# Kernel optimization log

Hardware: AMD Instinct MI355X
Metric: run time of the kernel (lower is better)

The kernel has to match this reference:

```python
import jax, jax.numpy as jnp
import numpy as np
from jax import lax

KX = jnp.array([[-1., 0., 1.], [-2., 0., 2.], [-1., 0., 1.]], dtype=jnp.float32)
KY = jnp.array([[1., 2., 1.], [0., 0., 0.], [-1., -2., -1.]], dtype=jnp.float32)


def _dwconv3(x, k):
    # x: [B,C,H,W]; k: [3,3]; depthwise 3x3 cross-correlation, padding=1 (matches torch F.conv2d)
    C = x.shape[1]
    kern = jnp.broadcast_to(k.astype(x.dtype)[None, None], (C, 1, 3, 3))
    return lax.conv_general_dilated(
        x, kern, window_strides=(1, 1), padding='SAME',
        dimension_numbers=('NCHW', 'OIHW', 'NCHW'), feature_group_count=C)


def _sobel(x):
    # |sobel_x| + |sobel_y|, shape [B,C,H,W] (the original adds a size-1 K dim, squeezed/kept trivially)
    return jnp.abs(_dwconv3(x, KX)) + jnp.abs(_dwconv3(x, KY))


def setup_inputs() -> dict:
    key = jax.random.key(0)
    ks = jax.random.split(key, 4)
    shape = (16, 1, 768, 768)
    return {
        'image_vis': jax.random.uniform(ks[0], shape, dtype=jnp.float32),
        'image_ir': jax.random.uniform(ks[1], shape, dtype=jnp.float32),
        'image_X': jax.random.uniform(ks[2], shape, dtype=jnp.float32),
        'image_Y': jax.random.uniform(ks[3], shape, dtype=jnp.float32),
    }


def reference(image_vis, image_ir, image_X, image_Y):
    # loss_in = mean(sobel(Y)^2) / mean(sobel(X)^2)
    x_size = jnp.mean(jnp.square(_sobel(image_X)))
    y_size = jnp.mean(jnp.square(_sobel(image_Y)))
    loss_in = y_size / x_size

    y_grad = _sobel(image_vis)
    ir_grad = _sobel(image_ir)          # broadcast replaces .expand
    gen_grad = _sobel(image_X)
    joint = jnp.maximum(y_grad, ir_grad)
    loss_grad = jnp.mean(jnp.abs(gen_grad - joint))  # F.l1_loss
    return (loss_in, loss_grad)
```

## Files before the change

### kernel.cpp

```cpp
#include <hip/hip_runtime.h>
#include <math.h>

#define IMG_H 768
#define IMG_W 768
#define BATCH 16
#define TH 4
#define TPB 256
#define NSTRIPS (IMG_H / TH)
#define NBLOCKS (NSTRIPS * BATCH)
#define NPIX ((size_t)BATCH * IMG_H * IMG_W)

typedef const __attribute__((address_space(1))) float* gp1_t;
typedef __attribute__((address_space(3))) float* lp3_t;

__global__ __launch_bounds__(TPB) void sobel_loss_main(
    const float* __restrict__ vis, const float* __restrict__ ir,
    const float* __restrict__ X, const float* __restrict__ Y,
    float* __restrict__ part)
{
    __shared__ __align__(16) float lds[4][TH + 2][IMG_W];
    __shared__ float red[3][4];

    const int tid  = threadIdx.x;
    const int lane = tid & 63;
    const int wv   = tid >> 6;
    const int y0   = blockIdx.x * TH;
    const size_t base = (size_t)blockIdx.y * (IMG_H * IMG_W);
    const int bid = blockIdx.y * NSTRIPS + blockIdx.x;

    const float* img[4] = { vis + base, ir + base, X + base, Y + base };

    {
        const float* ip = img[wv];
        #pragma unroll
        for (int i = 0; i < 3 * (TH + 2); ++i) {
            const int row = i / 3, seg = i % 3;
            int gr = y0 - 1 + row;
            int rc = gr < 0 ? 0 : (gr > IMG_H - 1 ? IMG_H - 1 : gr);
            const float* src = ip + (size_t)rc * IMG_W + seg * 256 + lane * 4;
            __builtin_amdgcn_global_load_lds((gp1_t)src, (lp3_t)&lds[wv][row][seg * 256], 16, 0, 0);
        }
    }
    __syncthreads();

    if (y0 == 0) {
        for (int i = tid; i < IMG_W; i += TPB) {
            lds[0][0][i] = 0.f; lds[1][0][i] = 0.f; lds[2][0][i] = 0.f; lds[3][0][i] = 0.f;
        }
        __syncthreads();
    } else if (y0 + TH == IMG_H) {
        for (int i = tid; i < IMG_W; i += TPB) {
            lds[0][TH + 1][i] = 0.f; lds[1][TH + 1][i] = 0.f; lds[2][TH + 1][i] = 0.f; lds[3][TH + 1][i] = 0.f;
        }
        __syncthreads();
    }

    const int r0 = wv, r1 = wv + 1, r2 = wv + 2;
    const int xb = lane * 12;

    float jnt[12];
    float sX2 = 0.f, sY2 = 0.f, sL1 = 0.f;

    #pragma unroll
    for (int im = 0; im < 4; ++im) {
        float4 t0 = *(const float4*)&lds[im][r0][xb];
        float4 t1 = *(const float4*)&lds[im][r0][xb + 4];
        float4 t2 = *(const float4*)&lds[im][r0][xb + 8];
        float4 m0 = *(const float4*)&lds[im][r1][xb];
        float4 m1 = *(const float4*)&lds[im][r1][xb + 4];
        float4 m2 = *(const float4*)&lds[im][r1][xb + 8];
        float4 b0 = *(const float4*)&lds[im][r2][xb];
        float4 b1 = *(const float4*)&lds[im][r2][xb + 4];
        float4 b2 = *(const float4*)&lds[im][r2][xb + 8];

        float T[14], M[14], B[14];
        T[1] = t0.x; T[2] = t0.y; T[3] = t0.z; T[4] = t0.w;
        T[5] = t1.x; T[6] = t1.y; T[7] = t1.z; T[8] = t1.w;
        T[9] = t2.x; T[10] = t2.y; T[11] = t2.z; T[12] = t2.w;
        M[1] = m0.x; M[2] = m0.y; M[3] = m0.z; M[4] = m0.w;
        M[5] = m1.x; M[6] = m1.y; M[7] = m1.z; M[8] = m1.w;
        M[9] = m2.x; M[10] = m2.y; M[11] = m2.z; M[12] = m2.w;
        B[1] = b0.x; B[2] = b0.y; B[3] = b0.z; B[4] = b0.w;
        B[5] = b1.x; B[6] = b1.y; B[7] = b1.z; B[8] = b1.w;
        B[9] = b2.x; B[10] = b2.y; B[11] = b2.z; B[12] = b2.w;

        float tl = __shfl_up(t2.w, 1),  tr = __shfl_down(t0.x, 1);
        float ml = __shfl_up(m2.w, 1),  mr = __shfl_down(m0.x, 1);
        float bl = __shfl_up(b2.w, 1),  br = __shfl_down(b0.x, 1);
        T[0] = (lane == 0) ? 0.f : tl;  T[13] = (lane == 63) ? 0.f : tr;
        M[0] = (lane == 0) ? 0.f : ml;  M[13] = (lane == 63) ? 0.f : mr;
        B[0] = (lane == 0) ? 0.f : bl;  B[13] = (lane == 63) ? 0.f : br;

        float s[14], d[14];
        #pragma unroll
        for (int j = 0; j < 14; ++j) { s[j] = T[j] + B[j]; d[j] = T[j] - B[j]; }

        float g[12];
        #pragma unroll
        for (int j = 0; j < 12; ++j) {
            float gx = (s[j + 2] - s[j]) + 2.f * (M[j + 2] - M[j]);
            float gy = d[j] + 2.f * d[j + 1] + d[j + 2];
            g[j] = fabsf(gx) + fabsf(gy);
        }

        if (im == 0) {
            #pragma unroll
            for (int j = 0; j < 12; ++j) jnt[j] = g[j];
        } else if (im == 1) {
            #pragma unroll
            for (int j = 0; j < 12; ++j) jnt[j] = fmaxf(jnt[j], g[j]);
        } else if (im == 2) {
            #pragma unroll
            for (int j = 0; j < 12; ++j) {
                sX2 += g[j] * g[j];
                sL1 += fabsf(g[j] - jnt[j]);
            }
        } else {
            #pragma unroll
            for (int j = 0; j < 12; ++j) sY2 += g[j] * g[j];
        }
    }

    #pragma unroll
    for (int off = 32; off > 0; off >>= 1) {
        sX2 += __shfl_down(sX2, off);
        sY2 += __shfl_down(sY2, off);
        sL1 += __shfl_down(sL1, off);
    }
    if (lane == 0) { red[0][wv] = sX2; red[1][wv] = sY2; red[2][wv] = sL1; }
    __syncthreads();
    if (tid == 0) {
        part[0 * NBLOCKS + bid] = red[0][0] + red[0][1] + red[0][2] + red[0][3];
        part[1 * NBLOCKS + bid] = red[1][0] + red[1][1] + red[1][2] + red[1][3];
        part[2 * NBLOCKS + bid] = red[2][0] + red[2][1] + red[2][2] + red[2][3];
    }
}

__global__ __launch_bounds__(1024) void reduce_finalize(
    const float* __restrict__ part, float* __restrict__ out)
{
    __shared__ float red[3][16];
    const int tid = threadIdx.x;

    float a = 0.f, b = 0.f, c = 0.f;
    for (int i = tid; i < NBLOCKS; i += 1024) {
        a += part[0 * NBLOCKS + i];
        b += part[1 * NBLOCKS + i];
        c += part[2 * NBLOCKS + i];
    }
    #pragma unroll
    for (int off = 32; off > 0; off >>= 1) {
        a += __shfl_down(a, off);
        b += __shfl_down(b, off);
        c += __shfl_down(c, off);
    }
    const int wave = tid >> 6;
    const int lane = tid & 63;
    if (lane == 0) { red[0][wave] = a; red[1][wave] = b; red[2][wave] = c; }
    __syncthreads();
    if (tid == 0) {
        float sa = 0.f, sb = 0.f, sc = 0.f;
        #pragma unroll
        for (int w = 0; w < 16; ++w) { sa += red[0][w]; sb += red[1][w]; sc += red[2][w]; }
        out[0] = sb / sa;
        out[1] = sc * (1.f / (float)NPIX);
    }
}

extern "C" void kernel_launch(void* const* d_in, const int* in_sizes, int n_in,
                              void* d_out, int out_size, void* d_ws, size_t ws_size,
                              hipStream_t stream) {
    const float* vis = (const float*)d_in[0];
    const float* ir  = (const float*)d_in[1];
    const float* X   = (const float*)d_in[2];
    const float* Y   = (const float*)d_in[3];
    float* out = (float*)d_out;
    float* part = (float*)d_ws;

    dim3 grid(NSTRIPS, BATCH);
    sobel_loss_main<<<grid, TPB, 0, stream>>>(vis, ir, X, Y, part);
    reduce_finalize<<<1, 1024, 0, stream>>>(part, out);
}
```

Baseline: 41.48 us.

## Persistent blocks with double-buffered LDS staging and fused last-block reduction

Replaces the one-strip-per-block grid with 256 persistent blocks that each process 12 strips. Staging uses two LDS buffers, so global-to-LDS loads for the next strip overlap computation on the current one, coordinated with manual vmcnt waits and barriers. The separate finalize kernel is replaced by an atomic counter, and the last finishing block performs the final reduction. This adds a memset launch and doubles LDS per block (about 147KB), which limits occupancy to one block per CU, and the inline waitcnt values have to be exactly right for correctness.

```diff
diff --git a/kernel.cpp b/kernel.cpp
--- a/kernel.cpp
+++ b/kernel.cpp
@@ -6,72 +6,48 @@
 #define BATCH 16
 #define TH 4
 #define TPB 256
-#define NSTRIPS (IMG_H / TH)
-#define NBLOCKS (NSTRIPS * BATCH)
+#define NBLK 256
+#define SPB 12
 #define NPIX ((size_t)BATCH * IMG_H * IMG_W)
 
 typedef const __attribute__((address_space(1))) float* gp1_t;
 typedef __attribute__((address_space(3))) float* lp3_t;
 
-__global__ __launch_bounds__(TPB) void sobel_loss_main(
-    const float* __restrict__ vis, const float* __restrict__ ir,
-    const float* __restrict__ X, const float* __restrict__ Y,
-    float* __restrict__ part)
-{
-    __shared__ __align__(16) float lds[4][TH + 2][IMG_W];
-    __shared__ float red[3][4];
-
-    const int tid  = threadIdx.x;
-    const int lane = tid & 63;
-    const int wv   = tid >> 6;
-    const int y0   = blockIdx.x * TH;
-    const size_t base = (size_t)blockIdx.y * (IMG_H * IMG_W);
-    const int bid = blockIdx.y * NSTRIPS + blockIdx.x;
-
-    const float* img[4] = { vis + base, ir + base, X + base, Y + base };
-
-    {
-        const float* ip = img[wv];
-        #pragma unroll
-        for (int i = 0; i < 3 * (TH + 2); ++i) {
-            const int row = i / 3, seg = i % 3;
-            int gr = y0 - 1 + row;
-            int rc = gr < 0 ? 0 : (gr > IMG_H - 1 ? IMG_H - 1 : gr);
-            const float* src = ip + (size_t)rc * IMG_W + seg * 256 + lane * 4;
-            __builtin_amdgcn_global_load_lds((gp1_t)src, (lp3_t)&lds[wv][row][seg * 256], 16, 0, 0);
-        }
-    }
-    __syncthreads();
-
-    if (y0 == 0) {
-        for (int i = tid; i < IMG_W; i += TPB) {
-            lds[0][0][i] = 0.f; lds[1][0][i] = 0.f; lds[2][0][i] = 0.f; lds[3][0][i] = 0.f;
-        }
-        __syncthreads();
-    } else if (y0 + TH == IMG_H) {
-        for (int i = tid; i < IMG_W; i += TPB) {
-            lds[0][TH + 1][i] = 0.f; lds[1][TH + 1][i] = 0.f; lds[2][TH + 1][i] = 0.f; lds[3][TH + 1][i] = 0.f;
-        }
-        __syncthreads();
-    }
-
+#define SBAR()   __builtin_amdgcn_s_barrier()
+#define SCHEDB() __builtin_amdgcn_sched_barrier(0)
+#define WAIT_VM18() asm volatile("s_waitcnt vmcnt(18)" ::: "memory")
+#define WAIT_VM0()  asm volatile("s_waitcnt vmcnt(0)"  ::: "memory")
+#define WAIT_LGKM0() asm volatile("s_waitcnt lgkmcnt(0)" ::: "memory")
+
+__device__ __forceinline__ void stage_img(const float* __restrict__ ip,
+                                          float (*buf)[IMG_W], int y0, int lane) {
+    #pragma unroll
+    for (int i = 0; i < 18; ++i) {
+        const int row = i / 3, seg = i % 3;
+        int gr = y0 - 1 + row;
+        int rc = gr < 0 ? 0 : (gr > IMG_H - 1 ? IMG_H - 1 : gr);
+        const float* src = ip + (size_t)rc * IMG_W + seg * 256 + lane * 4;
+        __builtin_amdgcn_global_load_lds((gp1_t)src, (lp3_t)&buf[row][seg * 256], 16, 0, 0);
+    }
+}
+
+__device__ __forceinline__ void compute_strip(const float (*buf)[TH + 2][IMG_W],
+                                              int wv, int lane,
+                                              float& sX2, float& sY2, float& sL1) {
     const int r0 = wv, r1 = wv + 1, r2 = wv + 2;
     const int xb = lane * 12;
-
     float jnt[12];
-    float sX2 = 0.f, sY2 = 0.f, sL1 = 0.f;
-
     #pragma unroll
     for (int im = 0; im < 4; ++im) {
-        float4 t0 = *(const float4*)&lds[im][r0][xb];
-        float4 t1 = *(const float4*)&lds[im][r0][xb + 4];
-        float4 t2 = *(const float4*)&lds[im][r0][xb + 8];
-        float4 m0 = *(const float4*)&lds[im][r1][xb];
-        float4 m1 = *(const float4*)&lds[im][r1][xb + 4];
-        float4 m2 = *(const float4*)&lds[im][r1][xb + 8];
-        float4 b0 = *(const float4*)&lds[im][r2][xb];
-        float4 b1 = *(const float4*)&lds[im][r2][xb + 4];
-        float4 b2 = *(const float4*)&lds[im][r2][xb + 8];
+        float4 t0 = *(const float4*)&buf[im][r0][xb];
+        float4 t1 = *(const float4*)&buf[im][r0][xb + 4];
+        float4 t2 = *(const float4*)&buf[im][r0][xb + 8];
+        float4 m0 = *(const float4*)&buf[im][r1][xb];
+        float4 m1 = *(const float4*)&buf[im][r1][xb + 4];
+        float4 m2 = *(const float4*)&buf[im][r1][xb + 8];
+        float4 b0 = *(const float4*)&buf[im][r2][xb];
+        float4 b1 = *(const float4*)&buf[im][r2][xb + 4];
+        float4 b2 = *(const float4*)&buf[im][r2][xb + 8];
 
         float T[14], M[14], B[14];
         T[1] = t0.x; T[2] = t0.y; T[3] = t0.z; T[4] = t0.w;
@@ -102,7 +78,6 @@
             float gy = d[j] + 2.f * d[j + 1] + d[j + 2];
             g[j] = fabsf(gx) + fabsf(gy);
         }
-
         if (im == 0) {
             #pragma unroll
             for (int j = 0; j < 12; ++j) jnt[j] = g[j];
@@ -111,14 +86,67 @@
             for (int j = 0; j < 12; ++j) jnt[j] = fmaxf(jnt[j], g[j]);
         } else if (im == 2) {
             #pragma unroll
-            for (int j = 0; j < 12; ++j) {
-                sX2 += g[j] * g[j];
-                sL1 += fabsf(g[j] - jnt[j]);
-            }
+            for (int j = 0; j < 12; ++j) { sX2 += g[j] * g[j]; sL1 += fabsf(g[j] - jnt[j]); }
         } else {
             #pragma unroll
             for (int j = 0; j < 12; ++j) sY2 += g[j] * g[j];
         }
+    }
+}
+
+__global__ __launch_bounds__(TPB) void sobel_loss_fused(
+    const float* __restrict__ vis, const float* __restrict__ ir,
+    const float* __restrict__ X, const float* __restrict__ Y,
+    float* __restrict__ part, unsigned* __restrict__ counter,
+    float* __restrict__ out)
+{
+    __shared__ __align__(16) float bufA[4][TH + 2][IMG_W];
+    __shared__ __align__(16) float bufB[4][TH + 2][IMG_W];
+    __shared__ float red[3][4];
+    __shared__ int lastLds;
+
+    const int tid  = threadIdx.x;
+    const int lane = tid & 63;
+    const int wv   = tid >> 6;
+    const int b    = blockIdx.x;
+    const int ib   = b >> 4;
+    const int ys0  = (b & 15) * SPB;
+    const size_t base = (size_t)ib * (IMG_H * IMG_W);
+    const float* img0[4] = { vis + base, ir + base, X + base, Y + base };
+    const float* ip = img0[wv];
+
+    float sX2 = 0.f, sY2 = 0.f, sL1 = 0.f;
+
+    stage_img(ip, bufA[wv], ys0 * TH, lane);
+
+    #pragma unroll 1
+    for (int t = 0; t < SPB / 2; ++t) {
+        const int y0A = (ys0 + 2 * t) * TH;
+        const int y0B = y0A + TH;
+
+        stage_img(ip, bufB[wv], y0B, lane);
+        WAIT_VM18();
+        SBAR(); SCHEDB();
+        if (y0A == 0) {
+            for (int i = tid; i < 4 * IMG_W; i += TPB) bufA[i / IMG_W][0][i % IMG_W] = 0.f;
+            WAIT_LGKM0(); SBAR();
+        }
+        compute_strip((const float (*)[TH + 2][IMG_W])bufA, wv, lane, sX2, sY2, sL1);
+        SCHEDB(); SBAR();
+
+        if (t < SPB / 2 - 1) {
+            stage_img(ip, bufA[wv], y0B + TH, lane);
+            WAIT_VM18();
+        } else {
+            WAIT_VM0();
+        }
+        SBAR(); SCHEDB();
+        if (y0B + TH == IMG_H) {
+            for (int i = tid; i < 4 * IMG_W; i += TPB) bufB[i / IMG_W][TH + 1][i % IMG_W] = 0.f;
+            WAIT_LGKM0(); SBAR();
+        }
+        compute_strip((const float (*)[TH + 2][IMG_W])bufB, wv, lane, sX2, sY2, sL1);
+        SCHEDB(); SBAR();
     }
 
     #pragma unroll
@@ -130,40 +158,35 @@
     if (lane == 0) { red[0][wv] = sX2; red[1][wv] = sY2; red[2][wv] = sL1; }
     __syncthreads();
     if (tid == 0) {
-        part[0 * NBLOCKS + bid] = red[0][0] + red[0][1] + red[0][2] + red[0][3];
-        part[1 * NBLOCKS + bid] = red[1][0] + red[1][1] + red[1][2] + red[1][3];
-        part[2 * NBLOCKS + bid] = red[2][0] + red[2][1] + red[2][2] + red[2][3];
-    }
-}
-
-__global__ __launch_bounds__(1024) void reduce_finalize(
-    const float* __restrict__ part, float* __restrict__ out)
-{
-    __shared__ float red[3][16];
-    const int tid = threadIdx.x;
-
-    float a = 0.f, b = 0.f, c = 0.f;
-    for (int i = tid; i < NBLOCKS; i += 1024) {
-        a += part[0 * NBLOCKS + i];
-        b += part[1 * NBLOCKS + i];
-        c += part[2 * NBLOCKS + i];
-    }
-    #pragma unroll
-    for (int off = 32; off > 0; off >>= 1) {
-        a += __shfl_down(a, off);
-        b += __shfl_down(b, off);
-        c += __shfl_down(c, off);
-    }
-    const int wave = tid >> 6;
-    const int lane = tid & 63;
-    if (lane == 0) { red[0][wave] = a; red[1][wave] = b; red[2][wave] = c; }
+        part[0 * NBLK + b] = red[0][0] + red[0][1] + red[0][2] + red[0][3];
+        part[1 * NBLK + b] = red[1][0] + red[1][1] + red[1][2] + red[1][3];
+        part[2 * NBLK + b] = red[2][0] + red[2][1] + red[2][2] + red[2][3];
+        __threadfence();
+        unsigned tk = atomicAdd(counter, 1u);
+        lastLds = (tk == NBLK - 1);
+    }
     __syncthreads();
-    if (tid == 0) {
-        float sa = 0.f, sb = 0.f, sc = 0.f;
+
+    if (lastLds) {
+        __threadfence();
+        float a = part[0 * NBLK + tid];
+        float c2 = part[1 * NBLK + tid];
+        float c3 = part[2 * NBLK + tid];
         #pragma unroll
-        for (int w = 0; w < 16; ++w) { sa += red[0][w]; sb += red[1][w]; sc += red[2][w]; }
-        out[0] = sb / sa;
-        out[1] = sc * (1.f / (float)NPIX);
+        for (int off = 32; off > 0; off >>= 1) {
+            a  += __shfl_down(a,  off);
+            c2 += __shfl_down(c2, off);
+            c3 += __shfl_down(c3, off);
+        }
+        if (lane == 0) { red[0][wv] = a; red[1][wv] = c2; red[2][wv] = c3; }
+        __syncthreads();
+        if (tid == 0) {
+            float sa = red[0][0] + red[0][1] + red[0][2] + red[0][3];
+            float sb = red[1][0] + red[1][1] + red[1][2] + red[1][3];
+            float sc = red[2][0] + red[2][1] + red[2][2] + red[2][3];
+            out[0] = sb / sa;
+            out[1] = sc * (1.f / (float)NPIX);
+        }
     }
 }
 
@@ -175,9 +198,10 @@
     const float* X   = (const float*)d_in[2];
     const float* Y   = (const float*)d_in[3];
     float* out = (float*)d_out;
-    float* part = (float*)d_ws;
-
-    dim3 grid(NSTRIPS, BATCH);
-    sobel_loss_main<<<grid, TPB, 0, stream>>>(vis, ir, X, Y, part);
-    reduce_finalize<<<1, 1024, 0, stream>>>(part, out);
-}
+
+    unsigned* counter = (unsigned*)d_ws;
+    float* part = (float*)((char*)d_ws + 256);
+
+    hipMemsetAsync(counter, 0, sizeof(unsigned), stream);
+    sobel_loss_fused<<<NBLK, TPB, 0, stream>>>(vis, ir, X, Y, part, counter, out);
+}
```

Measured after the change: 47.12 us. 13.6% more time.

## Fuse final reduction into main kernel via atomic counter and double strip height

Applied to the files above, without the earlier changes.

The separate finalize kernel is folded into the main kernel: each block writes its partial sums, bumps a global atomic counter, and the last block to finish reduces all partials and writes the outputs. Strip height goes from 4 to 8 rows with 512 threads per block, so the halo overhead per block is smaller and there are half as many blocks and partials. A memset of the counter is added before the launch. The larger LDS footprint (about 120 KB per block) may lower occupancy.

```diff
diff --git a/kernel.cpp b/kernel.cpp
--- a/kernel.cpp
+++ b/kernel.cpp
@@ -4,8 +4,8 @@
 #define IMG_H 768
 #define IMG_W 768
 #define BATCH 16
-#define TH 4
-#define TPB 256
+#define TH 8
+#define TPB 512
 #define NSTRIPS (IMG_H / TH)
 #define NBLOCKS (NSTRIPS * BATCH)
 #define NPIX ((size_t)BATCH * IMG_H * IMG_W)
@@ -13,13 +13,15 @@
 typedef const __attribute__((address_space(1))) float* gp1_t;
 typedef __attribute__((address_space(3))) float* lp3_t;
 
-__global__ __launch_bounds__(TPB) void sobel_loss_main(
+__global__ __launch_bounds__(TPB) void sobel_loss_fused(
     const float* __restrict__ vis, const float* __restrict__ ir,
     const float* __restrict__ X, const float* __restrict__ Y,
-    float* __restrict__ part)
+    float* __restrict__ part, unsigned* __restrict__ counter,
+    float* __restrict__ out)
 {
-    __shared__ __align__(16) float lds[4][TH + 2][IMG_W];
-    __shared__ float red[3][4];
+    __shared__ __align__(16) float buf[4][TH + 2][IMG_W];
+    __shared__ float red[3][8];
+    __shared__ int lastLds;
 
     const int tid  = threadIdx.x;
     const int lane = tid & 63;
@@ -28,30 +30,32 @@
     const size_t base = (size_t)blockIdx.y * (IMG_H * IMG_W);
     const int bid = blockIdx.y * NSTRIPS + blockIdx.x;
 
-    const float* img[4] = { vis + base, ir + base, X + base, Y + base };
-
     {
-        const float* ip = img[wv];
+        const int im = wv >> 1;
+        const float* ip = (im == 0) ? vis : (im == 1) ? ir : (im == 2) ? X : Y;
+        ip += base;
+        const int half = wv & 1;
         #pragma unroll
-        for (int i = 0; i < 3 * (TH + 2); ++i) {
-            const int row = i / 3, seg = i % 3;
+        for (int i = 0; i < 15; ++i) {
+            const int idx = half * 15 + i;
+            const int row = idx / 3, seg = idx % 3;
             int gr = y0 - 1 + row;
             int rc = gr < 0 ? 0 : (gr > IMG_H - 1 ? IMG_H - 1 : gr);
             const float* src = ip + (size_t)rc * IMG_W + seg * 256 + lane * 4;
-            __builtin_amdgcn_global_load_lds((gp1_t)src, (lp3_t)&lds[wv][row][seg * 256], 16, 0, 0);
+            __builtin_amdgcn_global_load_lds((gp1_t)src, (lp3_t)&buf[im][row][seg * 256], 16, 0, 0);
         }
     }
     __syncthreads();
 
-    if (y0 == 0) {
-        for (int i = tid; i < IMG_W; i += TPB) {
-            lds[0][0][i] = 0.f; lds[1][0][i] = 0.f; lds[2][0][i] = 0.f; lds[3][0][i] = 0.f;
-        }
+    if (blockIdx.x == 0) {
+        #pragma unroll
+        for (int im = 0; im < 4; ++im)
+            for (int i = tid; i < IMG_W; i += TPB) buf[im][0][i] = 0.f;
         __syncthreads();
-    } else if (y0 + TH == IMG_H) {
-        for (int i = tid; i < IMG_W; i += TPB) {
-            lds[0][TH + 1][i] = 0.f; lds[1][TH + 1][i] = 0.f; lds[2][TH + 1][i] = 0.f; lds[3][TH + 1][i] = 0.f;
-        }
+    } else if (blockIdx.x == NSTRIPS - 1) {
+        #pragma unroll
+        for (int im = 0; im < 4; ++im)
+            for (int i = tid; i < IMG_W; i += TPB) buf[im][TH + 1][i] = 0.f;
         __syncthreads();
     }
 
@@ -63,15 +67,15 @@
 
     #pragma unroll
     for (int im = 0; im < 4; ++im) {
-        float4 t0 = *(const float4*)&lds[im][r0][xb];
-        float4 t1 = *(const float4*)&lds[im][r0][xb + 4];
-        float4 t2 = *(const float4*)&lds[im][r0][xb + 8];
-        float4 m0 = *(const float4*)&lds[im][r1][xb];
-        float4 m1 = *(const float4*)&lds[im][r1][xb + 4];
-        float4 m2 = *(const float4*)&lds[im][r1][xb + 8];
-        float4 b0 = *(const float4*)&lds[im][r2][xb];
-        float4 b1 = *(const float4*)&lds[im][r2][xb + 4];
-        float4 b2 = *(const float4*)&lds[im][r2][xb + 8];
+        float4 t0 = *(const float4*)&buf[im][r0][xb];
+        float4 t1 = *(const float4*)&buf[im][r0][xb + 4];
+        float4 t2 = *(const float4*)&buf[im][r0][xb + 8];
+        float4 m0 = *(const float4*)&buf[im][r1][xb];
+        float4 m1 = *(const float4*)&buf[im][r1][xb + 4];
+        float4 m2 = *(const float4*)&buf[im][r1][xb + 8];
+        float4 b0 = *(const float4*)&buf[im][r2][xb];
+        float4 b1 = *(const float4*)&buf[im][r2][xb + 4];
+        float4 b2 = *(const float4*)&buf[im][r2][xb + 8];
 
         float T[14], M[14], B[14];
         T[1] = t0.x; T[2] = t0.y; T[3] = t0.z; T[4] = t0.w;
@@ -102,7 +106,6 @@
             float gy = d[j] + 2.f * d[j + 1] + d[j + 2];
             g[j] = fabsf(gx) + fabsf(gy);
         }
-
         if (im == 0) {
             #pragma unroll
             for (int j = 0; j < 12; ++j) jnt[j] = g[j];
@@ -111,10 +114,7 @@
             for (int j = 0; j < 12; ++j) jnt[j] = fmaxf(jnt[j], g[j]);
         } else if (im == 2) {
             #pragma unroll
-            for (int j = 0; j < 12; ++j) {
-                sX2 += g[j] * g[j];
-                sL1 += fabsf(g[j] - jnt[j]);
-            }
+            for (int j = 0; j < 12; ++j) { sX2 += g[j] * g[j]; sL1 += fabsf(g[j] - jnt[j]); }
         } else {
             #pragma unroll
             for (int j = 0; j < 12; ++j) sY2 += g[j] * g[j];
@@ -130,40 +130,43 @@
     if (lane == 0) { red[0][wv] = sX2; red[1][wv] = sY2; red[2][wv] = sL1; }
     __syncthreads();
     if (tid == 0) {
-        part[0 * NBLOCKS + bid] = red[0][0] + red[0][1] + red[0][2] + red[0][3];
-        part[1 * NBLOCKS + bid] = red[1][0] + red[1][1] + red[1][2] + red[1][3];
-        part[2 * NBLOCKS + bid] = red[2][0] + red[2][1] + red[2][2] + red[2][3];
+        float a = 0.f, b2 = 0.f, c = 0.f;
+        #pragma unroll
+        for (int w = 0; w < 8; ++w) { a += red[0][w]; b2 += red[1][w]; c += red[2][w]; }
+        part[0 * NBLOCKS + bid] = a;
+        part[1 * NBLOCKS + bid] = b2;
+        part[2 * NBLOCKS + bid] = c;
+        __threadfence();
+        unsigned tk = atomicAdd(counter, 1u);
+        lastLds = (tk == NBLOCKS - 1);
     }
-}
+    __syncthreads();
 
-__global__ __launch_bounds__(1024) void reduce_finalize(
-    const float* __restrict__ part, float* __restrict__ out)
-{
-    __shared__ float red[3][16];
-    const int tid = threadIdx.x;
-
-    float a = 0.f, b = 0.f, c = 0.f;
-    for (int i = tid; i < NBLOCKS; i += 1024) {
-        a += part[0 * NBLOCKS + i];
-        b += part[1 * NBLOCKS + i];
-        c += part[2 * NBLOCKS + i];
-    }
-    #pragma unroll
-    for (int off = 32; off > 0; off >>= 1) {
-        a += __shfl_down(a, off);
-        b += __shfl_down(b, off);
-        c += __shfl_down(c, off);
-    }
-    const int wave = tid >> 6;
-    const int lane = tid & 63;
-    if (lane == 0) { red[0][wave] = a; red[1][wave] = b; red[2][wave] = c; }
-    __syncthreads();
-    if (tid == 0) {
-        float sa = 0.f, sb = 0.f, sc = 0.f;
+    if (lastLds) {
+        __threadfence();
+        float a = 0.f, b2 = 0.f, c = 0.f;
         #pragma unroll
-        for (int w = 0; w < 16; ++w) { sa += red[0][w]; sb += red[1][w]; sc += red[2][w]; }
-        out[0] = sb / sa;
-        out[1] = sc * (1.f / (float)NPIX);
+        for (int k = 0; k < 3; ++k) {
+            int i = tid + k * TPB;
+            a  += part[0 * NBLOCKS + i];
+            b2 += part[1 * NBLOCKS + i];
+            c  += part[2 * NBLOCKS + i];
+        }
+        #pragma unroll
+        for (int off = 32; off > 0; off >>= 1) {
+            a  += __shfl_down(a,  off);
+            b2 += __shfl_down(b2, off);
+            c  += __shfl_down(c,  off);
+        }
+        if (lane == 0) { red[0][wv] = a; red[1][wv] = b2; red[2][wv] = c; }
+        __syncthreads();
+        if (tid == 0) {
+            float sa = 0.f, sb = 0.f, sc = 0.f;
+            #pragma unroll
+            for (int w = 0; w < 8; ++w) { sa += red[0][w]; sb += red[1][w]; sc += red[2][w]; }
+            out[0] = sb / sa;
+            out[1] = sc * (1.f / (float)NPIX);
+        }
     }
 }
 
@@ -175,9 +178,11 @@
     const float* X   = (const float*)d_in[2];
     const float* Y   = (const float*)d_in[3];
     float* out = (float*)d_out;
-    float* part = (float*)d_ws;
 
+    unsigned* counter = (unsigned*)d_ws;
+    float* part = (float*)((char*)d_ws + 256);
+
+    hipMemsetAsync(counter, 0, sizeof(unsigned), stream);
     dim3 grid(NSTRIPS, BATCH);
-    sobel_loss_main<<<grid, TPB, 0, stream>>>(vis, ir, X, Y, part);
-    reduce_finalize<<<1, 1024, 0, stream>>>(part, out);
+    sobel_loss_fused<<<grid, TPB, 0, stream>>>(vis, ir, X, Y, part, counter, out);
 }
```

Result: slower. 79.68 us (+92.1%).
